# Kernel optimization log

Measured on AMD Instinct MI355X. Metric: run time of the kernel, lower is better.

Reference implementation:

```python
import jax, jax.numpy as jnp
import numpy as np

D = 1024
N = 16
H = D // N  # 64
F = 4096
LOG2E = 1.442695041


def _rms_norm(x, scale, eps=1e-6):
    var = jnp.mean(x * x, axis=-1, keepdims=True)
    return x * jax.lax.rsqrt(var + eps) * scale


def _layer_norm(x, gamma, beta, eps=1e-5):
    m = jnp.mean(x, axis=-1, keepdims=True)
    v = jnp.mean(jnp.square(x - m), axis=-1, keepdims=True)
    return (x - m) * jax.lax.rsqrt(v + eps) * gamma + beta


def setup_inputs() -> dict:
    key = jax.random.key(0)
    ks = jax.random.split(key, 12)
    B, T = 8, 1024
    s = 0.02
    return {
        "x": jax.random.normal(ks[0], (B, T, D), dtype=jnp.float32),
        "padding": jnp.ones((B, T), dtype=jnp.float32),
        "rms_scale": jnp.ones((D,), dtype=jnp.float32),
        "per_dim_scale": jnp.zeros((H,), dtype=jnp.float32),
        "wq": jax.random.normal(ks[1], (D, N, H), dtype=jnp.float32) * s,
        "bq": jnp.zeros((N, H), dtype=jnp.float32),
        "wk": jax.random.normal(ks[2], (D, N, H), dtype=jnp.float32) * s,
        "bk": jnp.zeros((N, H), dtype=jnp.float32),
        "wv": jax.random.normal(ks[3], (D, N, H), dtype=jnp.float32) * s,
        "bv": jnp.zeros((N, H), dtype=jnp.float32),
        "wo": jax.random.normal(ks[4], (D, N, H), dtype=jnp.float32) * s,
        "bo": jnp.zeros((D,), dtype=jnp.float32),
        "ln_gamma": jnp.ones((D,), dtype=jnp.float32),
        "ln_beta": jnp.zeros((D,), dtype=jnp.float32),
        "w1": jax.random.normal(ks[5], (D, F), dtype=jnp.float32) * s,
        "b1": jnp.zeros((F,), dtype=jnp.float32),
        "w2": jax.random.normal(ks[6], (F, D), dtype=jnp.float32) * s,
        "b2": jnp.zeros((D,), dtype=jnp.float32),
    }


def reference(x, padding, rms_scale, per_dim_scale, wq, bq, wk, bk, wv, bv,
              wo, bo, ln_gamma, ln_beta, w1, b1, w2, b2):
    B, T, _ = x.shape
    res = x
    # pre-norm (RMS) for attention block
    xn = _rms_norm(x, rms_scale)
    # causal + padding mask: [B, T, S]
    causal = jnp.tril(jnp.ones((T, T), dtype=x.dtype))
    mask = causal[None, :, :] * padding[:, :, None] * padding[:, None, :]
    # projections: [B,T,N,H]
    q = jnp.einsum("btd,dnh->btnh", xn, wq) + bq
    k = jnp.einsum("btd,dnh->btnh", xn, wk) + bk
    v = jnp.einsum("btd,dnh->btnh", xn, wv) + bv
    # per-dim scale: (log2(e)/sqrt(H)) * softplus(p)
    scale = (LOG2E / jnp.sqrt(jnp.asarray(H, x.dtype))) * jax.nn.softplus(per_dim_scale)
    q = q * scale
    # scores: [B,N,T,S]
    dot = jnp.einsum("btnh,bsnh->bnts", q, k)
    dot = jnp.where(mask[:, None, :, :] == 0, jnp.asarray(-1e9, dot.dtype), dot)
    attn_w = jax.nn.softmax(dot, axis=-1)
    attn_out = jnp.einsum("bnts,bsnh->btnh", attn_w, v)
    attn = jnp.einsum("btnh,dnh->btd", attn_out, wo) + bo
    attn = res + attn
    # FFN block (pre-norm LayerNorm)
    res2 = attn
    h = _layer_norm(attn, ln_gamma, ln_beta)
    h = jax.nn.relu(h @ w1 + b1)
    h = h @ w2 + b2
    return res2 + h
```

## Files before the change

kernel.cpp:

```cpp
#include <hip/hip_runtime.h>
#include <hip/hip_bf16.h>
#include <cstdint>
#include <cstddef>

#define BB    8
#define TT    1024
#define DD    1024
#define NHEAD 16
#define HDIM  64
#define FF    4096

typedef unsigned short u16;
typedef unsigned int   u32;
typedef short bf16x8 __attribute__((ext_vector_type(8)));
typedef float floatx4 __attribute__((ext_vector_type(4)));
typedef float floatx16 __attribute__((ext_vector_type(16)));
typedef __attribute__((address_space(1))) const u32 gu32;
typedef __attribute__((address_space(3))) u32 lu32;

#define ZERO16 {0.f,0.f,0.f,0.f,0.f,0.f,0.f,0.f,0.f,0.f,0.f,0.f,0.f,0.f,0.f,0.f}

__device__ __forceinline__ float b2f(u16 u) {
  union { u32 i; float f; } c; c.i = ((u32)u) << 16; return c.f;
}
__device__ __forceinline__ u16 f2b(float f) {
  union { float f; u32 i; } c; c.f = f;
  u32 x = c.i;
  u32 r = (x + 0x7fffu + ((x >> 16) & 1u)) >> 16;
  return (u16)r;
}

__global__ __launch_bounds__(256) void rms_kernel(const float* __restrict__ x,
                                                  const float* __restrict__ g,
                                                  u16* __restrict__ xn) {
  int row = blockIdx.x;
  int tid = threadIdx.x;
  float4 v = ((const float4*)(x + (size_t)row * DD))[tid];
  float ss = v.x*v.x + v.y*v.y + v.z*v.z + v.w*v.w;
  for (int off = 32; off; off >>= 1) ss += __shfl_xor(ss, off);
  __shared__ float red[4];
  if ((tid & 63) == 0) red[tid >> 6] = ss;
  __syncthreads();
  float tot = red[0] + red[1] + red[2] + red[3];
  float inv = rsqrtf(tot * (1.0f / DD) + 1e-6f);
  float4 gv = ((const float4*)g)[tid];
  ushort4 o;
  o.x = f2b(v.x * inv * gv.x);
  o.y = f2b(v.y * inv * gv.y);
  o.z = f2b(v.z * inv * gv.z);
  o.w = f2b(v.w * inv * gv.w);
  ((ushort4*)(xn + (size_t)row * DD))[tid] = o;
}

__global__ __launch_bounds__(256) void ln_kernel(const float* __restrict__ a,
                                                 const float* __restrict__ g,
                                                 const float* __restrict__ be,
                                                 u16* __restrict__ o) {
  int row = blockIdx.x;
  int tid = threadIdx.x;
  float4 v = ((const float4*)(a + (size_t)row * DD))[tid];
  float s1 = v.x + v.y + v.z + v.w;
  float s2 = v.x*v.x + v.y*v.y + v.z*v.z + v.w*v.w;
  for (int off = 32; off; off >>= 1) {
    s1 += __shfl_xor(s1, off);
    s2 += __shfl_xor(s2, off);
  }
  __shared__ float r1[4], r2[4];
  if ((tid & 63) == 0) { r1[tid >> 6] = s1; r2[tid >> 6] = s2; }
  __syncthreads();
  float S1 = r1[0] + r1[1] + r1[2] + r1[3];
  float S2 = r2[0] + r2[1] + r2[2] + r2[3];
  float mean = S1 * (1.0f / DD);
  float var  = S2 * (1.0f / DD) - mean * mean;
  float inv  = rsqrtf(var + 1e-5f);
  float4 gv = ((const float4*)g)[tid];
  float4 bv = ((const float4*)be)[tid];
  ushort4 out;
  out.x = f2b((v.x - mean) * inv * gv.x + bv.x);
  out.y = f2b((v.y - mean) * inv * gv.y + bv.y);
  out.z = f2b((v.z - mean) * inv * gv.z + bv.z);
  out.w = f2b((v.w - mean) * inv * gv.w + bv.w);
  ((ushort4*)(o + (size_t)row * DD))[tid] = out;
}

__global__ void prep_kernel(const float* __restrict__ bq, const float* __restrict__ bk,
                            const float* __restrict__ bv, const float* __restrict__ pds,
                            float* __restrict__ bqkv, float* __restrict__ qsall) {
  int j = blockIdx.x * 1024 + threadIdx.x;
  float b = (j < 1024) ? bq[j] : (j < 2048) ? bk[j - 1024] : bv[j - 2048];
  bqkv[j] = b;
  float s = 1.f;
  if (j < 1024) {
    float p = pds[j & 63];
    float sp = (p > 0.f) ? (p + log1pf(__expf(-p))) : log1pf(__expf(p));
    s = 0.26017112252f * sp;
  }
  qsall[j] = s;
}

__global__ __launch_bounds__(256) void transpose_conv(const float* __restrict__ in,
                                                      u16* __restrict__ out,
                                                      int R, int C) {
  __shared__ float t[32][33];
  int bx = blockIdx.x * 32, by = blockIdx.y * 32;
  int tx = threadIdx.x & 31, ty = threadIdx.x >> 5;
#pragma unroll
  for (int i = 0; i < 32; i += 8)
    t[ty + i][tx] = in[(size_t)(by + ty + i) * C + bx + tx];
  __syncthreads();
#pragma unroll
  for (int i = 0; i < 32; i += 8)
    out[(size_t)(bx + ty + i) * R + by + tx] = f2b(t[tx][ty + i]);
}

__global__ __launch_bounds__(256) void conv_bf16(const float* __restrict__ in,
                                                 u16* __restrict__ out) {
  int i = blockIdx.x * 256 + threadIdx.x;
  float4 v = ((const float4*)in)[i];
  ushort4 o = { f2b(v.x), f2b(v.y), f2b(v.z), f2b(v.w) };
  ((ushort4*)out)[i] = o;
}

__global__ __launch_bounds__(256) void vtrans_kernel(const u16* __restrict__ vsrc,
                                                     u16* __restrict__ vdst) {
  __shared__ u16 tile[64][65];
  int bn = blockIdx.y; int b = bn >> 4, n = bn & 15;
  int t0 = blockIdx.x * 64;
  int tid = threadIdx.x;
  int rr = tid >> 4;
  int c4 = (tid & 15) * 4;
#pragma unroll
  for (int i = 0; i < 4; i++) {
    int r = i * 16 + rr;
    ushort4 d = *(const ushort4*)(vsrc + ((size_t)(b * TT + t0 + r)) * DD + n * HDIM + c4);
    tile[r][c4 + 0] = d.x; tile[r][c4 + 1] = d.y;
    tile[r][c4 + 2] = d.z; tile[r][c4 + 3] = d.w;
  }
  __syncthreads();
#pragma unroll
  for (int i = 0; i < 4; i++) {
    int h = i * 16 + rr;
    ushort4 d;
    d.x = tile[c4 + 0][h]; d.y = tile[c4 + 1][h];
    d.z = tile[c4 + 2][h]; d.w = tile[c4 + 3][h];
    *(ushort4*)(vdst + ((size_t)bn * HDIM + h) * TT + t0 + c4) = d;
  }
}

template <typename OUT_T>
__global__ __launch_bounds__(256) void mfma_gemm(
    const u16* __restrict__ A, const u16* __restrict__ Bt,
    const float* __restrict__ bias, const float* __restrict__ accsrc,
    const float* __restrict__ scale, OUT_T* __restrict__ C,
    int lda, int ldb, int K, int relu, int ldc, size_t regstride) {
  __shared__ u16 As[2][128 * 32] __attribute__((aligned(16)));
  __shared__ u16 Bs[2][128 * 32] __attribute__((aligned(16)));
  int tid = threadIdx.x;
  int lane = tid & 63;
  int wave = tid >> 6;
  int nbx = gridDim.x;
  int nwg = nbx * gridDim.y;
  int bid = blockIdx.y * nbx + blockIdx.x;
  int wid = (bid & 7) * (nwg >> 3) + (bid >> 3);
  int row0 = (wid / nbx) * 128, col0 = (wid % nbx) * 128;

  int sr = tid >> 2;
  int sk = (tid & 3) << 3;
  const u16* ag = A  + (size_t)(row0 + sr) * lda + sk;
  const u16* bg = Bt + (size_t)(col0 + sr) * ldb + sk;
  size_t rstepA = (size_t)64 * lda;
  size_t rstepB = (size_t)64 * ldb;

  int wr = (wave >> 1) * 64;
  int wc = (wave & 1) * 64;
  int fr = lane & 15;
  int fq = lane >> 4;

  floatx4 acc[4][4];
#pragma unroll
  for (int mi = 0; mi < 4; mi++)
#pragma unroll
    for (int ni = 0; ni < 4; ni++)
      acc[mi][ni] = (floatx4){0.f, 0.f, 0.f, 0.f};

  for (int k0 = 0; k0 < K; k0 += 64) {
#pragma unroll
    for (int kk = 0; kk < 2; kk++) {
      const u16* a_ = ag + kk * 32;
      const u16* b_ = bg + kk * 32;
      u16* asl = As[kk] + tid * 8;
      u16* bsl = Bs[kk] + tid * 8;
      __builtin_amdgcn_global_load_lds((gu32*)a_,            (lu32*)asl,          16, 0, 0);
      __builtin_amdgcn_global_load_lds((gu32*)(a_ + rstepA), (lu32*)(asl + 2048), 16, 0, 0);
      __builtin_amdgcn_global_load_lds((gu32*)b_,            (lu32*)bsl,          16, 0, 0);
      __builtin_amdgcn_global_load_lds((gu32*)(b_ + rstepB), (lu32*)(bsl + 2048), 16, 0, 0);
    }
    __syncthreads();
#pragma unroll
    for (int kk = 0; kk < 2; kk++) {
      const bf16x8* afp = (const bf16x8*)(As[kk] + (size_t)(wr + fr) * 32 + fq * 8);
      const bf16x8* bfp = (const bf16x8*)(Bs[kk] + (size_t)(wc + fr) * 32 + fq * 8);
      bf16x8 af[4], bf[4];
#pragma unroll
      for (int mi = 0; mi < 4; mi++) af[mi] = afp[mi * 64];
#pragma unroll
      for (int ni = 0; ni < 4; ni++) bf[ni] = bfp[ni * 64];
#pragma unroll
      for (int mi = 0; mi < 4; mi++)
#pragma unroll
        for (int ni = 0; ni < 4; ni++)
          acc[mi][ni] = __builtin_amdgcn_mfma_f32_16x16x32_bf16(
              af[mi], bf[ni], acc[mi][ni], 0, 0, 0);
    }
    __syncthreads();
    ag += 64; bg += 64;
  }

#pragma unroll
  for (int mi = 0; mi < 4; mi++) {
    int rbase = row0 + wr + mi * 16 + fq * 4;
#pragma unroll
    for (int ni = 0; ni < 4; ni++) {
      int col = col0 + wc + ni * 16 + fr;
      float bcol = bias ? bias[col] : 0.f;
      float scl  = scale ? scale[col] : 1.f;
      size_t cbase = regstride ? ((size_t)(col >> 10) * regstride + (col & 1023))
                               : (size_t)col;
#pragma unroll
      for (int reg = 0; reg < 4; reg++) {
        int r = rbase + reg;
        float v = (acc[mi][ni][reg] + bcol) * scl;
        if (relu)   v = fmaxf(v, 0.f);
        if (accsrc) v += accsrc[(size_t)r * ldc + col];
        if constexpr (sizeof(OUT_T) == 2) ((u16*)C)[cbase + (size_t)r * ldc] = f2b(v);
        else                              ((float*)C)[cbase + (size_t)r * ldc] = v;
      }
    }
  }
}

__global__ __launch_bounds__(256) void attn_mfma(
    const u16* __restrict__ q, const u16* __restrict__ k,
    const u16* __restrict__ vT, const float* __restrict__ padc,
    u16* __restrict__ ao) {
  int nwg = gridDim.x * gridDim.y;
  int bid = blockIdx.y * gridDim.x + blockIdx.x;
  int wid = (bid & 7) * (nwg >> 3) + (bid >> 3);
  int p  = wid & 3;
  int bn = wid >> 2;
  int b = bn >> 4, n = bn & 15;
  int tid = threadIdx.x;
  int w = tid >> 6, lane = tid & 63;
  int cl = lane & 31, hf = lane >> 5;
  __shared__ u16 Qs[128 * 64] __attribute__((aligned(16)));
  __shared__ u16 Ks[64 * 64]  __attribute__((aligned(16)));
  __shared__ u16 Vts[64 * 64] __attribute__((aligned(16)));
  __shared__ float padl[64];

  for (int half = 0; half < 2; half++) {
    int qt = half ? (7 - p) : p;
    int q0g = qt * 128;

#pragma unroll
    for (int it = 0; it < 4; it++) {
      int cid = it * 256 + tid; int r = cid >> 3, cc = cid & 7;
      uint4 d = *(const uint4*)(q + ((size_t)(b * TT + q0g + r)) * DD + n * HDIM + cc * 8);
      ((uint4*)Qs)[r * 8 + (cc ^ (r & 7))] = d;
    }
    __syncthreads();
    bf16x8 qf[4];
    int qrow = 32 * w + cl;
#pragma unroll
    for (int kc = 0; kc < 4; kc++)
      qf[kc] = ((const bf16x8*)Qs)[qrow * 8 + ((2 * kc + hf) ^ (cl & 7))];

    int tq = q0g + qrow;
    float prow = padc[b * TT + tq];
    bool prow_ok = (prow != 0.f);
    floatx16 o0 = ZERO16, o1 = ZERO16;
    float m_i = -INFINITY, l_i = 0.f;

    int jend = q0g + 128;
    for (int j0 = 0; j0 < jend; j0 += 64) {
#pragma unroll
      for (int it = 0; it < 2; it++) {
        int cid = it * 256 + tid; int r = cid >> 3, cc = cid & 7;
        uint4 dk = *(const uint4*)(k + ((size_t)(b * TT + j0 + r)) * DD + n * HDIM + cc * 8);
        ((uint4*)Ks)[r * 8 + (cc ^ (r & 7))] = dk;
        uint4 dv = *(const uint4*)(vT + ((size_t)(bn * HDIM + r)) * TT + j0 + cc * 8);
        ((uint4*)Vts)[r * 8 + (cc ^ (r & 7))] = dv;
      }
      if (tid < 64) padl[tid] = padc[b * TT + j0 + tid];
      __syncthreads();

      floatx16 s0 = ZERO16, s1 = ZERO16;
#pragma unroll
      for (int kc = 0; kc < 4; kc++) {
        bf16x8 ka0 = ((const bf16x8*)Ks)[cl * 8 + ((2 * kc + hf) ^ (cl & 7))];
        bf16x8 ka1 = ((const bf16x8*)Ks)[(32 + cl) * 8 + ((2 * kc + hf) ^ (cl & 7))];
        s0 = __builtin_amdgcn_mfma_f32_32x32x16_bf16(ka0, qf[kc], s0, 0, 0, 0);
        s1 = __builtin_amdgcn_mfma_f32_32x32x16_bf16(ka1, qf[kc], s1, 0, 0, 0);
      }

      float pl = padl[lane];
      bool fullt = (j0 + 63 <= q0g + 32 * w) && __all(pl != 0.f) && __all((int)prow_ok);
      float mloc = -INFINITY;
      if (fullt) {
#pragma unroll
        for (int i = 0; i < 16; i++)
          mloc = fmaxf(mloc, fmaxf(s0[i], s1[i]));
      } else {
#pragma unroll
        for (int q2 = 0; q2 < 2; q2++) {
#pragma unroll
          for (int rg = 0; rg < 4; rg++) {
            float4 pv = *(const float4*)&padl[q2 * 32 + rg * 8 + 4 * hf];
            int kb = j0 + q2 * 32 + rg * 8 + 4 * hf;
#pragma unroll
            for (int j = 0; j < 4; j++) {
              int idx = rg * 4 + j;
              float sval = q2 ? s1[idx] : s0[idx];
              float pvj = (j == 0) ? pv.x : (j == 1) ? pv.y : (j == 2) ? pv.z : pv.w;
              bool ok = prow_ok && (kb + j <= tq) && (pvj != 0.f);
              sval = ok ? sval : -1e9f;
              if (q2) s1[idx] = sval; else s0[idx] = sval;
              mloc = fmaxf(mloc, sval);
            }
          }
        }
      }
      float mtile = fmaxf(mloc, __shfl_xor(mloc, 32));
      float mnew = fmaxf(m_i, mtile);
      float alpha = exp2f(m_i - mnew);
      m_i = mnew;
      float ls = 0.f;
#pragma unroll
      for (int i = 0; i < 16; i++) {
        float p0 = exp2f(s0[i] - mnew); s0[i] = p0; ls += p0;
        float p1 = exp2f(s1[i] - mnew); s1[i] = p1; ls += p1;
      }
      ls += __shfl_xor(ls, 32);
      l_i = l_i * alpha + ls;
      o0 *= alpha; o1 *= alpha;

      u32 pk[8][2];
#pragma unroll
      for (int q2 = 0; q2 < 2; q2++)
#pragma unroll
        for (int rg = 0; rg < 4; rg++) {
          int be = q2 * 4 + rg;
          float a0 = q2 ? s1[rg * 4 + 0] : s0[rg * 4 + 0];
          float a1 = q2 ? s1[rg * 4 + 1] : s0[rg * 4 + 1];
          float a2 = q2 ? s1[rg * 4 + 2] : s0[rg * 4 + 2];
          float a3 = q2 ? s1[rg * 4 + 3] : s0[rg * 4 + 3];
          pk[be][0] = (u32)f2b(a0) | ((u32)f2b(a1) << 16);
          pk[be][1] = (u32)f2b(a2) | ((u32)f2b(a3) << 16);
        }
      u32 pp[8][2];
#pragma unroll
      for (int be = 0; be < 8; be++) {
        pp[be][0] = (u32)__shfl_xor((int)pk[be][0], 32);
        pp[be][1] = (u32)__shfl_xor((int)pk[be][1], 32);
      }

#pragma unroll
      for (int kc = 0; kc < 4; kc++) {
        union { u32 wd[4]; bf16x8 v; } pb;
        if (hf == 0) {
          pb.wd[0] = pk[2 * kc][0];     pb.wd[1] = pk[2 * kc][1];
          pb.wd[2] = pp[2 * kc][0];     pb.wd[3] = pp[2 * kc][1];
        } else {
          pb.wd[0] = pp[2 * kc + 1][0]; pb.wd[1] = pp[2 * kc + 1][1];
          pb.wd[2] = pk[2 * kc + 1][0]; pb.wd[3] = pk[2 * kc + 1][1];
        }
        bf16x8 vf0 = ((const bf16x8*)Vts)[cl * 8 + ((2 * kc + hf) ^ (cl & 7))];
        bf16x8 vf1 = ((const bf16x8*)Vts)[(32 + cl) * 8 + ((2 * kc + hf) ^ (cl & 7))];
        o0 = __builtin_amdgcn_mfma_f32_32x32x16_bf16(vf0, pb.v, o0, 0, 0, 0);
        o1 = __builtin_amdgcn_mfma_f32_32x32x16_bf16(vf1, pb.v, o1, 0, 0, 0);
      }
      __syncthreads();
    }

    float rl = 1.f / l_i;
#pragma unroll
    for (int hq = 0; hq < 2; hq++)
#pragma unroll
      for (int rg = 0; rg < 4; rg++) {
        ushort4 st;
        st.x = f2b((hq ? o1[rg * 4 + 0] : o0[rg * 4 + 0]) * rl);
        st.y = f2b((hq ? o1[rg * 4 + 1] : o0[rg * 4 + 1]) * rl);
        st.z = f2b((hq ? o1[rg * 4 + 2] : o0[rg * 4 + 2]) * rl);
        st.w = f2b((hq ? o1[rg * 4 + 3] : o0[rg * 4 + 3]) * rl);
        int col = n * HDIM + hq * 32 + rg * 8 + 4 * hf;
        *(ushort4*)(ao + ((size_t)(b * TT + tq)) * DD + col) = st;
      }
  }
}

extern "C" void kernel_launch(void* const* d_in, const int* in_sizes, int n_in,
                              void* d_out, int out_size, void* d_ws, size_t ws_size,
                              hipStream_t stream) {
  const float* x   = (const float*)d_in[0];
  const float* pad = (const float*)d_in[1];
  const float* rs  = (const float*)d_in[2];
  const float* pds = (const float*)d_in[3];
  const float* wq  = (const float*)d_in[4];
  const float* bq  = (const float*)d_in[5];
  const float* wk  = (const float*)d_in[6];
  const float* bk  = (const float*)d_in[7];
  const float* wv_ = (const float*)d_in[8];
  const float* bv  = (const float*)d_in[9];
  const float* wo  = (const float*)d_in[10];
  const float* bo  = (const float*)d_in[11];
  const float* lg  = (const float*)d_in[12];
  const float* lb  = (const float*)d_in[13];
  const float* w1  = (const float*)d_in[14];
  const float* b1  = (const float*)d_in[15];
  const float* w2  = (const float*)d_in[16];
  const float* b2  = (const float*)d_in[17];
  float* out = (float*)d_out;

  const size_t MB = (size_t)1 << 20;
  int G;
  if      (ws_size >= 88 * MB) G = 8;
  else if (ws_size >= 56 * MB) G = 4;
  else if (ws_size >= 40 * MB) G = 2;
  else                         G = 1;

  char* w = (char*)d_ws;
  u16* wqkvT = (u16*)(w);
  u16* woT   = (u16*)(w + 6 * MB);
  u16* w1T   = (u16*)(w + 8 * MB);
  u16* w2T   = (u16*)(w + 16 * MB);
  char* act = w + 24 * MB;
  const size_t SA = (size_t)2 * G * MB;
  u16*   regA = (u16*)act;
  u16*   qB   = (u16*)(act + SA);
  u16*   kC   = (u16*)(act + 2 * SA);
  u16*   vD   = (u16*)(act + 3 * SA);
  u16*   vTr  = regA;
  u16*   ao   = vD;
  u16*   hn   = regA;
  u16*   h1h  = qB;

  float* bqkv  = out + (size_t)out_size - 8192;
  float* qsall = bqkv + 3072;

  transpose_conv<<<dim3(32, 32),  256, 0, stream>>>(wq,  wqkvT,              DD, DD);
  transpose_conv<<<dim3(32, 32),  256, 0, stream>>>(wk,  wqkvT + 1024 * 1024, DD, DD);
  transpose_conv<<<dim3(32, 32),  256, 0, stream>>>(wv_, wqkvT + 2048 * 1024, DD, DD);
  conv_bf16<<<1024, 256, 0, stream>>>(wo, woT);
  transpose_conv<<<dim3(128, 32), 256, 0, stream>>>(w1, w1T, DD, FF);
  transpose_conv<<<dim3(32, 128), 256, 0, stream>>>(w2, w2T, FF, DD);
  prep_kernel<<<3, 1024, 0, stream>>>(bq, bk, bv, pds, bqkv, qsall);

  const int R = G * 1024;

  for (int c0 = 0; c0 < BB / G; c0++) {
    size_t rowoff = (size_t)c0 * R;
    const float* xc = x + rowoff * DD;
    float* outc = out + rowoff * DD;

    rms_kernel<<<R, 256, 0, stream>>>(xc, rs, regA);

    mfma_gemm<u16><<<dim3(24, R / 128), 256, 0, stream>>>(
        regA, wqkvT, bqkv, nullptr, qsall, qB,
        DD, DD, DD, 0, 1024, (size_t)R * 1024);

    vtrans_kernel<<<dim3(TT / 64, G * NHEAD), 256, 0, stream>>>(vD, vTr);

    attn_mfma<<<dim3(4, G * NHEAD), 256, 0, stream>>>(
        qB, kC, vTr, pad + rowoff, ao);

    mfma_gemm<float><<<dim3(8, R / 128), 256, 0, stream>>>(
        ao, woT, bo, xc, nullptr, outc, DD, DD, DD, 0, 1024, 0);

    ln_kernel<<<R, 256, 0, stream>>>(outc, lg, lb, hn);

    for (int f = 0; f < 2; f++) {
      mfma_gemm<u16><<<dim3(16, R / 128), 256, 0, stream>>>(
          hn, w1T + (size_t)f * 2048 * 1024, b1 + f * 2048, nullptr, nullptr,
          h1h, DD, DD, DD, 1, 2048, 0);
      mfma_gemm<float><<<dim3(8, R / 128), 256, 0, stream>>>(
          h1h, w2T + f * 2048, (f == 0) ? b2 : nullptr, outc, nullptr,
          outc, 2048, FF, 2048, 0, 1024, 0);
    }
  }
}
```

Measured before the change: 590.0 us.

## Add 256x256-tile triple-buffered MFMA GEMM for QKV and FFN1 projections

Introduces a new GEMM kernel with 256x256 output tiles, 512 threads (8 waves, each computing 128x64) and a three-stage LDS ring filled by direct global-to-LDS loads. This gives more operand reuse per byte loaded and deeper prefetch than the 128x128 double-buffered kernel. It is used for the QKV projection and the first FFN matmul. The cost is fewer workgroups, which may under-fill the GPU's compute units, and higher register and LDS pressure. A 96KB LDS footprint could also limit occupancy.

```diff
diff --git a/kernel.cpp b/kernel.cpp
--- a/kernel.cpp
+++ b/kernel.cpp
@@ -144,6 +144,109 @@
     d.x = tile[c4 + 0][h]; d.y = tile[c4 + 1][h];
     d.z = tile[c4 + 2][h]; d.w = tile[c4 + 3][h];
     *(ushort4*)(vdst + ((size_t)bn * HDIM + h) * TT + t0 + c4) = d;
+  }
+}
+
+template <typename OUT_T>
+__global__ __launch_bounds__(512, 2) void mfma_gemm256(
+    const u16* __restrict__ A, const u16* __restrict__ Bt,
+    const float* __restrict__ bias, const float* __restrict__ accsrc,
+    const float* __restrict__ scale, OUT_T* __restrict__ C,
+    int lda, int ldb, int K, int relu, int ldc, size_t regstride) {
+  __shared__ u16 As[3][256 * 32] __attribute__((aligned(16)));
+  __shared__ u16 Bs[3][256 * 32] __attribute__((aligned(16)));
+  int tid = threadIdx.x;
+  int lane = tid & 63;
+  int wv = tid >> 6;
+  int nbx = gridDim.x;
+  int nwg = nbx * gridDim.y;
+  int bid = blockIdx.y * nbx + blockIdx.x;
+  int wid = (bid & 7) * (nwg >> 3) + (bid >> 3);
+  int row0 = (wid / nbx) * 256, col0 = (wid % nbx) * 256;
+
+  int sr = tid >> 2;
+  int sk = (tid & 3) << 3;
+  const u16* ag = A  + (size_t)(row0 + sr) * lda + sk;
+  const u16* bg = Bt + (size_t)(col0 + sr) * ldb + sk;
+  size_t rstepA = (size_t)128 * lda;
+  size_t rstepB = (size_t)128 * ldb;
+
+  int fr = lane & 15, fq = lane >> 4;
+  int wr = (wv >> 2) * 128;
+  int wc = (wv & 3) * 64;
+
+  floatx4 acc[8][4];
+#pragma unroll
+  for (int mi = 0; mi < 8; mi++)
+#pragma unroll
+    for (int ni = 0; ni < 4; ni++)
+      acc[mi][ni] = (floatx4){0.f, 0.f, 0.f, 0.f};
+
+#define STAGE(tt)                                                              \
+  { int s_ = (tt) % 3;                                                         \
+    u16* asl = As[s_] + tid * 8;                                               \
+    u16* bsl = Bs[s_] + tid * 8;                                               \
+    const u16* a_ = ag + (size_t)(tt) * 32;                                    \
+    const u16* b_ = bg + (size_t)(tt) * 32;                                    \
+    __builtin_amdgcn_global_load_lds((gu32*)a_,            (lu32*)asl,          16, 0, 0); \
+    __builtin_amdgcn_global_load_lds((gu32*)(a_ + rstepA), (lu32*)(asl + 4096), 16, 0, 0); \
+    __builtin_amdgcn_global_load_lds((gu32*)b_,            (lu32*)bsl,          16, 0, 0); \
+    __builtin_amdgcn_global_load_lds((gu32*)(b_ + rstepB), (lu32*)(bsl + 4096), 16, 0, 0); }
+
+  int NT = K >> 5;
+  STAGE(0)
+  STAGE(1)
+
+  for (int t = 0; t < NT; ++t) {
+    if (t < NT - 1) asm volatile("s_waitcnt vmcnt(4)" ::: "memory");
+    else            asm volatile("s_waitcnt vmcnt(0)" ::: "memory");
+    asm volatile("s_barrier" ::: "memory");
+    if (t + 2 < NT) STAGE(t + 2)
+    int s = t % 3;
+    const u16* As_ = As[s];
+    const u16* Bs_ = Bs[s];
+    bf16x8 bf[4];
+#pragma unroll
+    for (int ni = 0; ni < 4; ni++)
+      bf[ni] = *(const bf16x8*)(Bs_ + (size_t)(wc + ni * 16 + fr) * 32 + fq * 8);
+    __builtin_amdgcn_s_setprio(1);
+#pragma unroll
+    for (int mh = 0; mh < 2; mh++) {
+      bf16x8 af[4];
+#pragma unroll
+      for (int mi = 0; mi < 4; mi++)
+        af[mi] = *(const bf16x8*)(As_ + (size_t)(wr + mh * 64 + mi * 16 + fr) * 32 + fq * 8);
+#pragma unroll
+      for (int mi = 0; mi < 4; mi++)
+#pragma unroll
+        for (int ni = 0; ni < 4; ni++)
+          acc[mh * 4 + mi][ni] = __builtin_amdgcn_mfma_f32_16x16x32_bf16(
+              af[mi], bf[ni], acc[mh * 4 + mi][ni], 0, 0, 0);
+    }
+    __builtin_amdgcn_s_setprio(0);
+  }
+#undef STAGE
+
+#pragma unroll
+  for (int mi = 0; mi < 8; mi++) {
+    int rbase = row0 + wr + mi * 16 + fq * 4;
+#pragma unroll
+    for (int ni = 0; ni < 4; ni++) {
+      int col = col0 + wc + ni * 16 + fr;
+      float bcol = bias ? bias[col] : 0.f;
+      float scl  = scale ? scale[col] : 1.f;
+      size_t cbase = regstride ? ((size_t)(col >> 10) * regstride + (col & 1023))
+                               : (size_t)col;
+#pragma unroll
+      for (int reg = 0; reg < 4; reg++) {
+        int r = rbase + reg;
+        float v = (acc[mi][ni][reg] + bcol) * scl;
+        if (relu)   v = fmaxf(v, 0.f);
+        if (accsrc) v += accsrc[(size_t)r * ldc + col];
+        if constexpr (sizeof(OUT_T) == 2) ((u16*)C)[cbase + (size_t)r * ldc] = f2b(v);
+        else                              ((float*)C)[cbase + (size_t)r * ldc] = v;
+      }
+    }
   }
 }
 
@@ -463,7 +566,7 @@
 
     rms_kernel<<<R, 256, 0, stream>>>(xc, rs, regA);
 
-    mfma_gemm<u16><<<dim3(24, R / 128), 256, 0, stream>>>(
+    mfma_gemm256<u16><<<dim3(12, R / 256), 512, 0, stream>>>(
         regA, wqkvT, bqkv, nullptr, qsall, qB,
         DD, DD, DD, 0, 1024, (size_t)R * 1024);
 
@@ -478,7 +581,7 @@
     ln_kernel<<<R, 256, 0, stream>>>(outc, lg, lb, hn);
 
     for (int f = 0; f < 2; f++) {
-      mfma_gemm<u16><<<dim3(16, R / 128), 256, 0, stream>>>(
+      mfma_gemm256<u16><<<dim3(8, R / 256), 512, 0, stream>>>(
           hn, w1T + (size_t)f * 2048 * 1024, b1 + f * 2048, nullptr, nullptr,
           h1h, DD, DD, DD, 1, 2048, 0);
       mfma_gemm<float><<<dim3(8, R / 128), 256, 0, stream>>>(
```

Measured after the change: 618.2 us. +4.8%, slower.
